# Optimization experiments

Measured on AMD Instinct MI355X. Metric: run time of the kernel, lower is better.

## Reference

```python
import jax, jax.numpy as jnp
import numpy as np

B, N, C_IN, F, OUT = 32, 1000, 128, 128, 64
RATIOS = (0.8, 0.8)


def setup_inputs() -> dict:
    key = jax.random.key(0)
    ks = jax.random.split(key, 10)
    N_nodes = jax.random.randint(ks[0], (B,), 500, N + 1, dtype=jnp.int32)
    ar = jnp.arange(N)
    mask = (ar[None, :] < N_nodes[:, None]).astype(jnp.float32)  # [B,N]
    A = (jax.random.uniform(ks[1], (B, N, N)) < 0.02).astype(jnp.float32)
    A = A * (1.0 - jnp.eye(N, dtype=jnp.float32))
    A = jnp.maximum(A, A.transpose(0, 2, 1))  # symmetric, no self loops
    A = A * mask[:, :, None] * mask[:, None, :]
    x = jax.random.normal(ks[2], (B, N, C_IN)) * mask[..., None]

    def lin(k, fin, fout):
        bnd = 1.0 / np.sqrt(fin)
        kw, kb = jax.random.split(k)
        W = jax.random.uniform(kw, (fout, fin), minval=-bnd, maxval=bnd)
        b = jax.random.uniform(kb, (fout,), minval=-bnd, maxval=bnd)
        return W, b

    W0, b0 = lin(ks[3], C_IN, F)
    W1, b1 = lin(ks[4], F, F)
    W2, b2 = lin(ks[5], F, F)
    bnd = 1.0 / np.sqrt(F)
    p0 = jax.random.uniform(ks[6], (F, 1), minval=-bnd, maxval=bnd)
    p1 = jax.random.uniform(ks[7], (F, 1), minval=-bnd, maxval=bnd)
    Wfc, bfc = lin(ks[8], F, OUT)
    return dict(x=x, A=A, mask=mask, N_nodes=N_nodes,
                W0=W0, b0=b0, W1=W1, b1=b1, W2=W2, b2=b2,
                p0=p0, p1=p1, Wfc=Wfc, bfc=bfc)


def _gconv(x, A, mask, W, b):
    # K=1 Kipf-Welling conv: L = D^-1/2 (A+I) D^-1/2; relu(Linear(L x)) * mask
    n = A.shape[1]
    A_hat = A + jnp.eye(n, dtype=A.dtype)
    D = (jnp.sum(A_hat, axis=1) + 1e-5) ** -0.5  # [B,N]
    L = D[:, :, None] * A_hat * D[:, None, :]
    h = jnp.einsum('bij,bjc->bic', L, x)
    h = h @ W.T + b
    return jax.nn.relu(h) * mask[..., None]


def _pool(x, A, mask, N_nodes, p, ratio):
    # score each node, drop the N_remove lowest-scoring valid nodes per graph
    y = (x @ p)[..., 0] / jnp.sqrt(jnp.sum(p ** 2))  # [B,N]
    N_remove = (N_nodes.astype(jnp.float32) * (1.0 - ratio)).astype(jnp.int32)
    y_key = jnp.where(mask > 0, y, jnp.inf)  # invalid nodes rank last
    ranks = jnp.argsort(jnp.argsort(y_key, axis=1), axis=1)  # ascending rank
    new_mask = ((ranks >= N_remove[:, None]) & (mask > 0)).astype(x.dtype)
    x = x * jnp.tanh(y)[..., None] * new_mask[..., None]
    A = new_mask[:, :, None] * A * new_mask[:, None, :]
    return x, A, new_mask, N_nodes - N_remove


def reference(x, A, mask, N_nodes, W0, b0, W1, b1, W2, b2, p0, p1, Wfc, bfc):
    h = _gconv(x, A, mask, W0, b0)
    h, A1, m1, n1 = _pool(h, A, mask, N_nodes, p0, RATIOS[0])
    h = _gconv(h, A1, m1, W1, b1)
    h, A2, m2, n2 = _pool(h, A1, m1, n1, p1, RATIOS[1])
    h = _gconv(h, A2, m2, W2, b2)
    g = jnp.max(h, axis=1)  # [B,F] global max pool
    return g @ Wfc.T + bfc  # [B,OUT]
```

## Files before the change

### kernel.cpp

```cpp
#include <hip/hip_runtime.h>
#include <math.h>

#define BB 32
#define NN 1000
#define CC 128
#define FF 128
#define OO 64
#define CAP 128
#define NB 40

#define RMC ((float)(1.0 - 0.8))

__global__ void k_pre(const float* __restrict__ mask, const int* __restrict__ Nn,
                      const float* __restrict__ p0, const float* __restrict__ p1,
                      const float* __restrict__ W0, const float* __restrict__ W1,
                      const float* __restrict__ W2,
                      float* __restrict__ m, int* __restrict__ ncur0,
                      float* __restrict__ pn, float* __restrict__ gate,
                      float* __restrict__ Wt){
  int blk = blockIdx.x, tid = threadIdx.x;
  if (blk == 3){
    for (int i = tid; i < BB*NN; i += 256){ float v = mask[i]; m[i] = v; gate[i] = v; }
    if (tid < BB) ncur0[tid] = Nn[tid];
    if (tid == 64){ float s=0.f; for(int c=0;c<FF;c++) s += p0[c]*p0[c]; pn[0] = sqrtf(s); }
    if (tid == 65){ float s=0.f; for(int c=0;c<FF;c++) s += p1[c]*p1[c]; pn[1] = sqrtf(s); }
  } else {
    const float* W = (blk == 0) ? W0 : (blk == 1) ? W1 : W2;
    float* T = Wt + (size_t)blk*FF*CC;
    for (int e = tid; e < FF*CC; e += 256){
      int c = e >> 7, f = e & 127;
      T[e] = W[f*CC + c];
    }
  }
}

__global__ void k_csr(const float* __restrict__ A, short* __restrict__ idx,
                      int* __restrict__ cnt){
  int i = blockIdx.x, b = blockIdx.y, lane = threadIdx.x;
  const float4* row = (const float4*)(A + ((size_t)b*NN + i)*NN);
  short* out = idx + ((size_t)b*NN + i)*CAP;
  int count = 0;
  for (int base = 0; base < 250; base += 64){
    int q = base + lane;
    float4 v;
    if (q < 250) v = row[q]; else { v.x=v.y=v.z=v.w=0.f; }
    int lc = (v.x!=0.f) + (v.y!=0.f) + (v.z!=0.f) + (v.w!=0.f);
    int pre = lc;
    #pragma unroll
    for (int off = 1; off < 64; off <<= 1){
      int t = __shfl_up(pre, off);
      if (lane >= off) pre += t;
    }
    int tot = __shfl(pre, 63);
    pre -= lc;
    int slot = count + pre;
    int j = q*4;
    if (v.x!=0.f && slot < CAP) out[slot++] = (short)j;
    if (v.y!=0.f && slot < CAP) out[slot++] = (short)(j+1);
    if (v.z!=0.f && slot < CAP) out[slot++] = (short)(j+2);
    if (v.w!=0.f && slot < CAP) out[slot++] = (short)(j+3);
    count += tot;
  }
  if (lane == 0) cnt[b*NN + i] = (count < CAP) ? count : CAP;
}

__global__ void k_deg(const short* __restrict__ idx, const int* __restrict__ cnt,
                      const float* __restrict__ m, float* __restrict__ D){
  __shared__ float ml[NN];
  int b = blockIdx.y, tid = threadIdx.x;
  for (int i = tid; i < NN; i += 256) ml[i] = m[b*NN + i];
  __syncthreads();
  int j = blockIdx.x*250 + tid;
  if (tid < 250){
    const short* r = idx + ((size_t)b*NN + j)*CAP;
    int n = cnt[b*NN + j];
    float s0=0.f, s1=0.f, s2=0.f, s3=0.f;
    int k = 0;
    for (; k+4 <= n; k += 4){
      s0 += ml[r[k]]; s1 += ml[r[k+1]]; s2 += ml[r[k+2]]; s3 += ml[r[k+3]];
    }
    for (; k < n; k++) s0 += ml[r[k]];
    D[b*NN + j] = 1.0f / sqrtf(((s0+s1)+(s2+s3)) + 1.0f + 1e-5f);
  }
}

__global__ void k_agg(const short* __restrict__ idx, const int* __restrict__ cnt,
                      const float* __restrict__ D, const float* __restrict__ gate,
                      const float* __restrict__ m,
                      const float* __restrict__ h, float* __restrict__ Y){
  __shared__ int   nb[CAP];
  __shared__ float dn[CAP];
  int blk = blockIdx.x;
  int b = (blk & 7) + 8*((blk >> 3) & 3);
  int i = blk >> 5;
  if (m[b*NN + i] == 0.f) return;
  int c = threadIdx.x;
  int n = cnt[b*NN + i];
  int np = (n + 7) & ~7;
  const short* r = idx + ((size_t)b*NN + i)*CAP;
  for (int k = c; k < np; k += 128){
    int j = (k < n) ? (int)r[k] : 0;
    nb[k] = j*CC;
    dn[k] = (k < n) ? D[b*NN + j] * gate[b*NN + j] : 0.f;
  }
  __syncthreads();
  float a0=0.f,a1=0.f,a2=0.f,a3=0.f,a4=0.f,a5=0.f,a6=0.f,a7=0.f;
  const float* hb = h + (size_t)b*NN*CC;
  for (int k = 0; k < np; k += 8){
    float v0 = hb[nb[k+0] + c];
    float v1 = hb[nb[k+1] + c];
    float v2 = hb[nb[k+2] + c];
    float v3 = hb[nb[k+3] + c];
    float v4 = hb[nb[k+4] + c];
    float v5 = hb[nb[k+5] + c];
    float v6 = hb[nb[k+6] + c];
    float v7 = hb[nb[k+7] + c];
    a0 += dn[k+0]*v0; a1 += dn[k+1]*v1;
    a2 += dn[k+2]*v2; a3 += dn[k+3]*v3;
    a4 += dn[k+4]*v4; a5 += dn[k+5]*v5;
    a6 += dn[k+6]*v6; a7 += dn[k+7]*v7;
  }
  Y[((size_t)b*NN + i)*CC + c] = ((a0+a1)+(a2+a3)) + ((a4+a5)+(a6+a7));
}

__global__ void k_lin(const float* __restrict__ Y, const float* __restrict__ h,
                      const float* __restrict__ Dv, const float* __restrict__ m,
                      const float* __restrict__ gate,
                      const float* __restrict__ Wt,
                      const float* __restrict__ bias, float* __restrict__ Hout){
  __shared__ float t[NB][CC];
  int b = blockIdx.y, tid = threadIdx.x;
  int i0 = blockIdx.x * NB;
  for (int e = tid; e < NB*CC; e += 256){
    int n = e >> 7, c = e & 127;
    int i = i0 + n;
    float Di = Dv[b*NN + i], mi = m[b*NN + i], gi = gate[b*NN + i];
    size_t o = ((size_t)b*NN + i)*CC + c;
    t[n][c] = Di*(mi*Y[o]) + Di*Di*(gi*h[o]);
  }
  __syncthreads();
  int fg = tid & 31;
  int nr = tid >> 5;
  float acc[5][4];
  float4 bi = ((const float4*)bias)[fg];
  #pragma unroll
  for (int n5 = 0; n5 < 5; n5++){
    acc[n5][0]=bi.x; acc[n5][1]=bi.y; acc[n5][2]=bi.z; acc[n5][3]=bi.w;
  }
  for (int c4 = 0; c4 < 32; c4++){
    float4 tv[5];
    #pragma unroll
    for (int n5 = 0; n5 < 5; n5++)
      tv[n5] = *((const float4*)&t[nr + n5*8][c4*4]);
    #pragma unroll
    for (int k = 0; k < 4; k++){
      float4 wv = ((const float4*)Wt)[(size_t)(c4*4 + k)*32 + fg];
      #pragma unroll
      for (int n5 = 0; n5 < 5; n5++){
        float tvv = (k==0) ? tv[n5].x : (k==1) ? tv[n5].y : (k==2) ? tv[n5].z : tv[n5].w;
        acc[n5][0] += tvv*wv.x; acc[n5][1] += tvv*wv.y;
        acc[n5][2] += tvv*wv.z; acc[n5][3] += tvv*wv.w;
      }
    }
  }
  #pragma unroll
  for (int n5 = 0; n5 < 5; n5++){
    int i = i0 + nr + n5*8;
    float mi = m[b*NN + i];
    float4 o4;
    o4.x = fmaxf(acc[n5][0], 0.f)*mi;
    o4.y = fmaxf(acc[n5][1], 0.f)*mi;
    o4.z = fmaxf(acc[n5][2], 0.f)*mi;
    o4.w = fmaxf(acc[n5][3], 0.f)*mi;
    ((float4*)&Hout[((size_t)b*NN + i)*CC])[fg] = o4;
  }
}

__global__ void k_score(const float* __restrict__ H, const float* __restrict__ p,
                        const float* __restrict__ pn, float* __restrict__ y){
  int i = blockIdx.x, b = blockIdx.y, lane = threadIdx.x;
  const float* hrow = H + ((size_t)b*NN + i)*CC;
  float s = hrow[lane]*p[lane] + hrow[lane+64]*p[lane+64];
  for (int off = 32; off > 0; off >>= 1) s += __shfl_down(s, off);
  if (lane == 0) y[b*NN + i] = s / pn[0];
}

__global__ void k_pool(const float* __restrict__ y, float* __restrict__ m,
                       const int* __restrict__ ncur_in, int* __restrict__ ncur_out,
                       float* __restrict__ gate){
  __shared__ float yk[NN];
  int b = blockIdx.y, tid = threadIdx.x;
  int i = blockIdx.x*256 + tid;
  for (int j = tid; j < NN; j += 256)
    yk[j] = (m[b*NN + j] > 0.f) ? y[b*NN + j] : INFINITY;
  __syncthreads();
  int n = ncur_in[b];
  int nr = (int)((float)n * RMC);
  float myv = (i < NN) ? yk[i] : INFINITY;
  int cnt = 0;
  const float4* yk4 = (const float4*)yk;
  #pragma unroll 5
  for (int q = 0; q < 250; q++){
    float4 v = yk4[q];
    int j0 = q*4;
    cnt += (int)((v.x < myv) || (v.x == myv && j0     < i));
    cnt += (int)((v.y < myv) || (v.y == myv && j0 + 1 < i));
    cnt += (int)((v.z < myv) || (v.z == myv && j0 + 2 < i));
    cnt += (int)((v.w < myv) || (v.w == myv && j0 + 3 < i));
  }
  if (i < NN){
    bool keep = (cnt >= nr) && (m[b*NN + i] > 0.f);
    m[b*NN + i]    = keep ? 1.0f : 0.0f;
    gate[b*NN + i] = keep ? tanhf(y[b*NN + i]) : 0.0f;
  }
  if (blockIdx.x == 0 && tid == 0) ncur_out[b] = n - nr;
}

__global__ void k_fmax(const float* __restrict__ H, const float* __restrict__ m,
                       float* __restrict__ part){
  int sx = blockIdx.x, b = blockIdx.y, c = threadIdx.x;
  float mx = 0.f;
  int i0 = sx*125;
  for (int i = i0; i < i0+125; i++){
    if (m[b*NN + i] != 0.f)
      mx = fmaxf(mx, H[((size_t)b*NN + i)*CC + c]);
  }
  part[((size_t)b*8 + sx)*CC + c] = mx;
}

__global__ void k_fc(const float* __restrict__ part, const float* __restrict__ Wfc,
                     const float* __restrict__ bfc, float* __restrict__ out){
  __shared__ float g[FF];
  int b = blockIdx.x, tid = threadIdx.x;
  float mx = 0.f;
  #pragma unroll
  for (int s = 0; s < 8; s++) mx = fmaxf(mx, part[((size_t)b*8 + s)*CC + tid]);
  g[tid] = mx;
  __syncthreads();
  if (tid < OO){
    float acc = bfc[tid];
    for (int c = 0; c < FF; c++) acc += g[c]*Wfc[tid*FF + c];
    out[b*OO + tid] = acc;
  }
}

extern "C" void kernel_launch(void* const* d_in, const int* in_sizes, int n_in,
                              void* d_out, int out_size, void* d_ws, size_t ws_size,
                              hipStream_t stream) {
  const float* x    = (const float*)d_in[0];
  const float* A    = (const float*)d_in[1];
  const float* mask = (const float*)d_in[2];
  const int*   Nn   = (const int*)  d_in[3];
  const float* W0   = (const float*)d_in[4];
  const float* b0   = (const float*)d_in[5];
  const float* W1   = (const float*)d_in[6];
  const float* b1   = (const float*)d_in[7];
  const float* W2   = (const float*)d_in[8];
  const float* b2   = (const float*)d_in[9];
  const float* p0   = (const float*)d_in[10];
  const float* p1   = (const float*)d_in[11];
  const float* Wfc  = (const float*)d_in[12];
  const float* bfc  = (const float*)d_in[13];
  float* out = (float*)d_out;

  char* w = (char*)d_ws;
  float* H   = (float*)w; w += (size_t)BB*NN*CC*4;
  float* Yb  = (float*)w; w += (size_t)BB*NN*CC*4;
  short* idx = (short*)w; w += (size_t)BB*NN*CAP*2;
  float* Wt  = (float*)w; w += (size_t)3*FF*CC*4;
  float* part= (float*)w; w += (size_t)8*BB*CC*4;
  int*   cnt = (int*)w;   w += (size_t)BB*NN*4;
  float* D   = (float*)w; w += (size_t)BB*NN*4;
  float* m   = (float*)w; w += (size_t)BB*NN*4;
  float* ysc = (float*)w; w += (size_t)BB*NN*4;
  float* gate= (float*)w; w += (size_t)BB*NN*4;
  int*   ncur= (int*)w;   w += 3*BB*sizeof(int);
  float* pn  = (float*)w; w += 64;

  k_pre<<<4, 256, 0, stream>>>(mask, Nn, p0, p1, W0, W1, W2, m, ncur, pn, gate, Wt);
  k_csr<<<dim3(NN, BB), 64, 0, stream>>>(A, idx, cnt);

  k_deg<<<dim3(4, BB), 256, 0, stream>>>(idx, cnt, m, D);
  k_agg<<<BB*NN, 128, 0, stream>>>(idx, cnt, D, gate, m, x, Yb);
  k_lin<<<dim3(25, BB), 256, 0, stream>>>(Yb, x, D, m, gate, Wt + 0*FF*CC, b0, H);
  k_score<<<dim3(NN, BB), 64, 0, stream>>>(H, p0, pn + 0, ysc);
  k_pool<<<dim3(4, BB), 256, 0, stream>>>(ysc, m, ncur + 0*BB, ncur + 1*BB, gate);

  k_deg<<<dim3(4, BB), 256, 0, stream>>>(idx, cnt, m, D);
  k_agg<<<BB*NN, 128, 0, stream>>>(idx, cnt, D, gate, m, H, Yb);
  k_lin<<<dim3(25, BB), 256, 0, stream>>>(Yb, H, D, m, gate, Wt + 1*FF*CC, b1, H);
  k_score<<<dim3(NN, BB), 64, 0, stream>>>(H, p1, pn + 1, ysc);
  k_pool<<<dim3(4, BB), 256, 0, stream>>>(ysc, m, ncur + 1*BB, ncur + 2*BB, gate);

  k_deg<<<dim3(4, BB), 256, 0, stream>>>(idx, cnt, m, D);
  k_agg<<<BB*NN, 128, 0, stream>>>(idx, cnt, D, gate, m, H, Yb);
  k_lin<<<dim3(25, BB), 256, 0, stream>>>(Yb, H, D, m, gate, Wt + 2*FF*CC, b2, H);

  k_fmax<<<dim3(8, BB), 128, 0, stream>>>(H, m, part);
  k_fc<<<BB, 128, 0, stream>>>(part, Wfc, bfc, out);
}
```

Measured before the change: 512.9 us.

## Fuse degree computation into CSR and pooling, move normalization into aggregation

Computes the first-layer degree normalization directly in the CSR build kernel (using the raw neighbor count, since the initial adjacency is already masked). Folds the per-layer degree kernel into a single-block-per-graph pooling kernel. Precomputes D*gate per node so the aggregation gather reads one value instead of two. Moves the D_i scaling and self-loop term into the aggregation kernel so the linear kernel only does a plain float4 tile load. It also widens the gather unroll to 16 and removes three launches. In exchange, pooling now runs as 32 blocks of 1024 threads, which lowers parallelism there, and the aggregation kernel must write zero rows for masked nodes.

```diff
diff --git a/kernel.cpp b/kernel.cpp
--- a/kernel.cpp
+++ b/kernel.cpp
@@ -15,13 +15,13 @@
                       const float* __restrict__ p0, const float* __restrict__ p1,
                       const float* __restrict__ W0, const float* __restrict__ W1,
                       const float* __restrict__ W2,
-                      float* __restrict__ m, int* __restrict__ ncur0,
+                      float* __restrict__ m, int* __restrict__ ncur,
                       float* __restrict__ pn, float* __restrict__ gate,
                       float* __restrict__ Wt){
   int blk = blockIdx.x, tid = threadIdx.x;
   if (blk == 3){
     for (int i = tid; i < BB*NN; i += 256){ float v = mask[i]; m[i] = v; gate[i] = v; }
-    if (tid < BB) ncur0[tid] = Nn[tid];
+    if (tid < BB) ncur[tid] = Nn[tid];
     if (tid == 64){ float s=0.f; for(int c=0;c<FF;c++) s += p0[c]*p0[c]; pn[0] = sqrtf(s); }
     if (tid == 65){ float s=0.f; for(int c=0;c<FF;c++) s += p1[c]*p1[c]; pn[1] = sqrtf(s); }
   } else {
@@ -34,8 +34,9 @@
   }
 }
 
-__global__ void k_csr(const float* __restrict__ A, short* __restrict__ idx,
-                      int* __restrict__ cnt){
+__global__ void k_csr(const float* __restrict__ A, const float* __restrict__ mask,
+                      short* __restrict__ idx, int* __restrict__ cnt,
+                      float* __restrict__ D, float* __restrict__ dg){
   int i = blockIdx.x, b = blockIdx.y, lane = threadIdx.x;
   const float4* row = (const float4*)(A + ((size_t)b*NN + i)*NN);
   short* out = idx + ((size_t)b*NN + i)*CAP;
@@ -61,83 +62,66 @@
     if (v.w!=0.f && slot < CAP) out[slot++] = (short)(j+3);
     count += tot;
   }
-  if (lane == 0) cnt[b*NN + i] = (count < CAP) ? count : CAP;
-}
-
-__global__ void k_deg(const short* __restrict__ idx, const int* __restrict__ cnt,
-                      const float* __restrict__ m, float* __restrict__ D){
-  __shared__ float ml[NN];
-  int b = blockIdx.y, tid = threadIdx.x;
-  for (int i = tid; i < NN; i += 256) ml[i] = m[b*NN + i];
-  __syncthreads();
-  int j = blockIdx.x*250 + tid;
-  if (tid < 250){
-    const short* r = idx + ((size_t)b*NN + j)*CAP;
-    int n = cnt[b*NN + j];
-    float s0=0.f, s1=0.f, s2=0.f, s3=0.f;
-    int k = 0;
-    for (; k+4 <= n; k += 4){
-      s0 += ml[r[k]]; s1 += ml[r[k+1]]; s2 += ml[r[k+2]]; s3 += ml[r[k+3]];
-    }
-    for (; k < n; k++) s0 += ml[r[k]];
-    D[b*NN + j] = 1.0f / sqrtf(((s0+s1)+(s2+s3)) + 1.0f + 1e-5f);
-  }
-}
-
-__global__ void k_agg(const short* __restrict__ idx, const int* __restrict__ cnt,
-                      const float* __restrict__ D, const float* __restrict__ gate,
-                      const float* __restrict__ m,
-                      const float* __restrict__ h, float* __restrict__ Y){
+  if (lane == 0){
+    cnt[b*NN + i] = (count < CAP) ? count : CAP;
+    float Dv = 1.0f / sqrtf((float)count + 1.0f + 1e-5f);
+    D[b*NN + i]  = Dv;
+    dg[b*NN + i] = Dv * mask[b*NN + i];
+  }
+}
+
+__global__ void k_aggt(const short* __restrict__ idx, const int* __restrict__ cnt,
+                       const float* __restrict__ D, const float* __restrict__ dg,
+                       const float* __restrict__ m, const float* __restrict__ gate,
+                       const float* __restrict__ h, float* __restrict__ T){
   __shared__ int   nb[CAP];
   __shared__ float dn[CAP];
   int blk = blockIdx.x;
   int b = (blk & 7) + 8*((blk >> 3) & 3);
   int i = blk >> 5;
-  if (m[b*NN + i] == 0.f) return;
   int c = threadIdx.x;
+  size_t orow = ((size_t)b*NN + i)*CC;
+  if (m[b*NN + i] == 0.f){
+    T[orow + c] = 0.f;
+    return;
+  }
   int n = cnt[b*NN + i];
-  int np = (n + 7) & ~7;
+  int np = (n + 15) & ~15;
   const short* r = idx + ((size_t)b*NN + i)*CAP;
   for (int k = c; k < np; k += 128){
     int j = (k < n) ? (int)r[k] : 0;
     nb[k] = j*CC;
-    dn[k] = (k < n) ? D[b*NN + j] * gate[b*NN + j] : 0.f;
-  }
-  __syncthreads();
-  float a0=0.f,a1=0.f,a2=0.f,a3=0.f,a4=0.f,a5=0.f,a6=0.f,a7=0.f;
+    dn[k] = (k < n) ? dg[b*NN + j] : 0.f;
+  }
+  __syncthreads();
+  float acc[16];
+  #pragma unroll
+  for (int q = 0; q < 16; q++) acc[q] = 0.f;
   const float* hb = h + (size_t)b*NN*CC;
-  for (int k = 0; k < np; k += 8){
-    float v0 = hb[nb[k+0] + c];
-    float v1 = hb[nb[k+1] + c];
-    float v2 = hb[nb[k+2] + c];
-    float v3 = hb[nb[k+3] + c];
-    float v4 = hb[nb[k+4] + c];
-    float v5 = hb[nb[k+5] + c];
-    float v6 = hb[nb[k+6] + c];
-    float v7 = hb[nb[k+7] + c];
-    a0 += dn[k+0]*v0; a1 += dn[k+1]*v1;
-    a2 += dn[k+2]*v2; a3 += dn[k+3]*v3;
-    a4 += dn[k+4]*v4; a5 += dn[k+5]*v5;
-    a6 += dn[k+6]*v6; a7 += dn[k+7]*v7;
-  }
-  Y[((size_t)b*NN + i)*CC + c] = ((a0+a1)+(a2+a3)) + ((a4+a5)+(a6+a7));
-}
-
-__global__ void k_lin(const float* __restrict__ Y, const float* __restrict__ h,
-                      const float* __restrict__ Dv, const float* __restrict__ m,
-                      const float* __restrict__ gate,
+  for (int k = 0; k < np; k += 16){
+    float v[16];
+    #pragma unroll
+    for (int q = 0; q < 16; q++) v[q] = hb[nb[k+q] + c];
+    #pragma unroll
+    for (int q = 0; q < 16; q++) acc[q] += dn[k+q]*v[q];
+  }
+  float Y = (((acc[0]+acc[1])+(acc[2]+acc[3])) + ((acc[4]+acc[5])+(acc[6]+acc[7])))
+          + (((acc[8]+acc[9])+(acc[10]+acc[11])) + ((acc[12]+acc[13])+(acc[14]+acc[15])));
+  float Di = D[b*NN + i];
+  float gi = gate[b*NN + i];
+  T[orow + c] = Di*Y + Di*Di*(gi*hb[(size_t)i*CC + c]);
+}
+
+__global__ void k_lin(const float* __restrict__ T, const float* __restrict__ m,
                       const float* __restrict__ Wt,
                       const float* __restrict__ bias, float* __restrict__ Hout){
   __shared__ float t[NB][CC];
   int b = blockIdx.y, tid = threadIdx.x;
   int i0 = blockIdx.x * NB;
-  for (int e = tid; e < NB*CC; e += 256){
-    int n = e >> 7, c = e & 127;
-    int i = i0 + n;
-    float Di = Dv[b*NN + i], mi = m[b*NN + i], gi = gate[b*NN + i];
-    size_t o = ((size_t)b*NN + i)*CC + c;
-    t[n][c] = Di*(mi*Y[o]) + Di*Di*(gi*h[o]);
-  }
+  const float4* Tg = (const float4*)(T + ((size_t)b*NN + i0)*CC);
+  float4* tl = (float4*)&t[0][0];
+  #pragma unroll
+  for (int e = 0; e < 5; e++) tl[tid + e*256] = Tg[tid + e*256];
   __syncthreads();
   int fg = tid & 31;
   int nr = tid >> 5;
@@ -185,35 +169,53 @@
   if (lane == 0) y[b*NN + i] = s / pn[0];
 }
 
-__global__ void k_pool(const float* __restrict__ y, float* __restrict__ m,
-                       const int* __restrict__ ncur_in, int* __restrict__ ncur_out,
-                       float* __restrict__ gate){
+__global__ void k_poold(const float* __restrict__ y, const short* __restrict__ idx,
+                        const int* __restrict__ cnt, float* __restrict__ m,
+                        int* __restrict__ ncur, float* __restrict__ gate,
+                        float* __restrict__ D, float* __restrict__ dg){
   __shared__ float yk[NN];
-  int b = blockIdx.y, tid = threadIdx.x;
-  int i = blockIdx.x*256 + tid;
-  for (int j = tid; j < NN; j += 256)
-    yk[j] = (m[b*NN + j] > 0.f) ? y[b*NN + j] : INFINITY;
-  __syncthreads();
-  int n = ncur_in[b];
+  __shared__ float ml[NN];
+  int b = blockIdx.x, tid = threadIdx.x;
+  if (tid < NN) yk[tid] = (m[b*NN + tid] > 0.f) ? y[b*NN + tid] : INFINITY;
+  __syncthreads();
+  int n = ncur[b];
   int nr = (int)((float)n * RMC);
-  float myv = (i < NN) ? yk[i] : INFINITY;
-  int cnt = 0;
+  float myv = (tid < NN) ? yk[tid] : INFINITY;
+  int cntr = 0;
   const float4* yk4 = (const float4*)yk;
   #pragma unroll 5
   for (int q = 0; q < 250; q++){
     float4 v = yk4[q];
     int j0 = q*4;
-    cnt += (int)((v.x < myv) || (v.x == myv && j0     < i));
-    cnt += (int)((v.y < myv) || (v.y == myv && j0 + 1 < i));
-    cnt += (int)((v.z < myv) || (v.z == myv && j0 + 2 < i));
-    cnt += (int)((v.w < myv) || (v.w == myv && j0 + 3 < i));
-  }
-  if (i < NN){
-    bool keep = (cnt >= nr) && (m[b*NN + i] > 0.f);
-    m[b*NN + i]    = keep ? 1.0f : 0.0f;
-    gate[b*NN + i] = keep ? tanhf(y[b*NN + i]) : 0.0f;
-  }
-  if (blockIdx.x == 0 && tid == 0) ncur_out[b] = n - nr;
+    cntr += (int)((v.x < myv) || (v.x == myv && j0     < tid));
+    cntr += (int)((v.y < myv) || (v.y == myv && j0 + 1 < tid));
+    cntr += (int)((v.z < myv) || (v.z == myv && j0 + 2 < tid));
+    cntr += (int)((v.w < myv) || (v.w == myv && j0 + 3 < tid));
+  }
+  float gv = 0.f, keepf = 0.f;
+  if (tid < NN){
+    bool keep = (cntr >= nr) && (m[b*NN + tid] > 0.f);
+    keepf = keep ? 1.0f : 0.0f;
+    gv = keep ? tanhf(y[b*NN + tid]) : 0.0f;
+    m[b*NN + tid]    = keepf;
+    gate[b*NN + tid] = gv;
+    ml[tid] = keepf;
+  }
+  __syncthreads();
+  if (tid < NN){
+    const short* r = idx + ((size_t)b*NN + tid)*CAP;
+    int nc = cnt[b*NN + tid];
+    float s0=0.f, s1=0.f, s2=0.f, s3=0.f;
+    int k = 0;
+    for (; k+4 <= nc; k += 4){
+      s0 += ml[r[k]]; s1 += ml[r[k+1]]; s2 += ml[r[k+2]]; s3 += ml[r[k+3]];
+    }
+    for (; k < nc; k++) s0 += ml[r[k]];
+    float Dv = 1.0f / sqrtf(((s0+s1)+(s2+s3)) + 1.0f + 1e-5f);
+    D[b*NN + tid]  = Dv;
+    dg[b*NN + tid] = Dv * gv;
+  }
+  if (tid == 0) ncur[b] = n - nr;
 }
 
 __global__ void k_fmax(const float* __restrict__ H, const float* __restrict__ m,
@@ -265,7 +267,7 @@
 
   char* w = (char*)d_ws;
   float* H   = (float*)w; w += (size_t)BB*NN*CC*4;
-  float* Yb  = (float*)w; w += (size_t)BB*NN*CC*4;
+  float* T   = (float*)w; w += (size_t)BB*NN*CC*4;
   short* idx = (short*)w; w += (size_t)BB*NN*CAP*2;
   float* Wt  = (float*)w; w += (size_t)3*FF*CC*4;
   float* part= (float*)w; w += (size_t)8*BB*CC*4;
@@ -274,27 +276,25 @@
   float* m   = (float*)w; w += (size_t)BB*NN*4;
   float* ysc = (float*)w; w += (size_t)BB*NN*4;
   float* gate= (float*)w; w += (size_t)BB*NN*4;
-  int*   ncur= (int*)w;   w += 3*BB*sizeof(int);
+  float* dg  = (float*)w; w += (size_t)BB*NN*4;
+  int*   ncur= (int*)w;   w += BB*sizeof(int);
   float* pn  = (float*)w; w += 64;
 
   k_pre<<<4, 256, 0, stream>>>(mask, Nn, p0, p1, W0, W1, W2, m, ncur, pn, gate, Wt);
-  k_csr<<<dim3(NN, BB), 64, 0, stream>>>(A, idx, cnt);
-
-  k_deg<<<dim3(4, BB), 256, 0, stream>>>(idx, cnt, m, D);
-  k_agg<<<BB*NN, 128, 0, stream>>>(idx, cnt, D, gate, m, x, Yb);
-  k_lin<<<dim3(25, BB), 256, 0, stream>>>(Yb, x, D, m, gate, Wt + 0*FF*CC, b0, H);
+  k_csr<<<dim3(NN, BB), 64, 0, stream>>>(A, mask, idx, cnt, D, dg);
+
+  k_aggt<<<BB*NN, 128, 0, stream>>>(idx, cnt, D, dg, m, gate, x, T);
+  k_lin<<<dim3(25, BB), 256, 0, stream>>>(T, m, Wt + 0*FF*CC, b0, H);
   k_score<<<dim3(NN, BB), 64, 0, stream>>>(H, p0, pn + 0, ysc);
-  k_pool<<<dim3(4, BB), 256, 0, stream>>>(ysc, m, ncur + 0*BB, ncur + 1*BB, gate);
-
-  k_deg<<<dim3(4, BB), 256, 0, stream>>>(idx, cnt, m, D);
-  k_agg<<<BB*NN, 128, 0, stream>>>(idx, cnt, D, gate, m, H, Yb);
-  k_lin<<<dim3(25, BB), 256, 0, stream>>>(Yb, H, D, m, gate, Wt + 1*FF*CC, b1, H);
+  k_poold<<<BB, 1024, 0, stream>>>(ysc, idx, cnt, m, ncur, gate, D, dg);
+
+  k_aggt<<<BB*NN, 128, 0, stream>>>(idx, cnt, D, dg, m, gate, H, T);
+  k_lin<<<dim3(25, BB), 256, 0, stream>>>(T, m, Wt + 1*FF*CC, b1, H);
   k_score<<<dim3(NN, BB), 64, 0, stream>>>(H, p1, pn + 1, ysc);
-  k_pool<<<dim3(4, BB), 256, 0, stream>>>(ysc, m, ncur + 1*BB, ncur + 2*BB, gate);
-
-  k_deg<<<dim3(4, BB), 256, 0, stream>>>(idx, cnt, m, D);
-  k_agg<<<BB*NN, 128, 0, stream>>>(idx, cnt, D, gate, m, H, Yb);
-  k_lin<<<dim3(25, BB), 256, 0, stream>>>(Yb, H, D, m, gate, Wt + 2*FF*CC, b2, H);
+  k_poold<<<BB, 1024, 0, stream>>>(ysc, idx, cnt, m, ncur, gate, D, dg);
+
+  k_aggt<<<BB*NN, 128, 0, stream>>>(idx, cnt, D, dg, m, gate, H, T);
+  k_lin<<<dim3(25, BB), 256, 0, stream>>>(T, m, Wt + 2*FF*CC, b2, H);
 
   k_fmax<<<dim3(8, BB), 128, 0, stream>>>(H, m, part);
   k_fc<<<BB, 128, 0, stream>>>(part, Wfc, bfc, out);
```

After: 536.0 us. 1.04x slower.
